# Kernel optimization log

Hardware: AMD Instinct MI355X
Metric: run time of the kernel (lower is better)

The kernel has to match this reference:

```python
import jax, jax.numpy as jnp
import numpy as np

N_NODES = 50000
N_EDGES = 800000
D_IN, D_HID, D_OUT = 128, 256, 256


def _sage_conv(x, src, dst, w_l, b_l, w_r, n_nodes):
    # PyG SAGEConv (mean aggr): out = lin_l(mean_{j in N(i)} x_j) + lin_r(x_i)
    # lin_l has bias, lin_r has no bias.
    msg_sum = jax.ops.segment_sum(x[src], dst, num_segments=n_nodes)  # [N, d]
    deg = jax.ops.segment_sum(jnp.ones_like(dst, dtype=x.dtype), dst, num_segments=n_nodes)
    agg = msg_sum / jnp.maximum(deg, 1.0)[:, None]
    return agg @ w_l.T + b_l + x @ w_r.T


def setup_inputs() -> dict:
    key = jax.random.key(0)
    ks = jax.random.split(key, 8)
    x = jax.random.normal(ks[0], (N_NODES, D_IN), dtype=jnp.float32)
    edge_index = jax.random.randint(ks[1], (2, N_EDGES), 0, N_NODES, dtype=jnp.int64)
    s1 = 1.0 / np.sqrt(D_IN)
    s2 = 1.0 / np.sqrt(D_HID)
    w_l1 = jax.random.uniform(ks[2], (D_HID, D_IN), jnp.float32, -s1, s1)
    b_l1 = jax.random.uniform(ks[3], (D_HID,), jnp.float32, -s1, s1)
    w_r1 = jax.random.uniform(ks[4], (D_HID, D_IN), jnp.float32, -s1, s1)
    w_l2 = jax.random.uniform(ks[5], (D_OUT, D_HID), jnp.float32, -s2, s2)
    b_l2 = jax.random.uniform(ks[6], (D_OUT,), jnp.float32, -s2, s2)
    w_r2 = jax.random.uniform(ks[7], (D_OUT, D_HID), jnp.float32, -s2, s2)
    return {"x": x, "edge_index": edge_index,
            "w_l1": w_l1, "b_l1": b_l1, "w_r1": w_r1,
            "w_l2": w_l2, "b_l2": b_l2, "w_r2": w_r2}


def reference(x, edge_index, w_l1, b_l1, w_r1, w_l2, b_l2, w_r2):
    src, dst = edge_index[0], edge_index[1]
    h = jax.nn.relu(_sage_conv(x, src, dst, w_l1, b_l1, w_r1, N_NODES))
    out = jax.nn.relu(_sage_conv(h, src, dst, w_l2, b_l2, w_r2, N_NODES))
    return out
```

## Files before the change

### kernel.cpp

```cpp
#include <hip/hip_runtime.h>
#include <hip/hip_fp16.h>
#include <stdint.h>

#define N_NODES 50000
#define N_EDGES 800000
#define BCAP 64
#define NPART 782
#define NSUB 16
#define SCAP 128

typedef _Float16 f16x8 __attribute__((ext_vector_type(8)));
typedef __attribute__((ext_vector_type(4))) float f32x4;

__device__ __forceinline__ unsigned short f2h(float f) {
    return __builtin_bit_cast(unsigned short, (_Float16)f);
}

__device__ __forceinline__ unsigned char f2fp8o(float v) {
    v = fminf(v, 440.f) + 0.015625f;
    unsigned int u = __builtin_bit_cast(unsigned int, v);
    u += 0x7FFFFu + ((u >> 20) & 1u);
    return (unsigned char)((u >> 20) - 960u);
}

__device__ __forceinline__ void load_lds16(const void* g, void* l) {
    __builtin_amdgcn_global_load_lds(
        (const __attribute__((address_space(1))) void*)(uintptr_t)g,
        (__attribute__((address_space(3))) void*)(unsigned int)(uintptr_t)l,
        16, 0, 0);
}

__global__ __launch_bounds__(256) void part_append_k(
    const int* __restrict__ src, const int* __restrict__ dst,
    int* __restrict__ pcnt, unsigned int* __restrict__ pbuf, int nedges)
{
    int t = blockIdx.x * 256 + threadIdx.x;
    int e0 = t * 4;
    if (e0 >= nedges) return;
    int4 s4 = *(const int4*)(src + e0);
    int4 d4 = *(const int4*)(dst + e0);

    int c0 = (d4.x >> 6) * NSUB + ((e0 + 0) & (NSUB - 1));
    int c1 = (d4.y >> 6) * NSUB + ((e0 + 1) & (NSUB - 1));
    int c2 = (d4.z >> 6) * NSUB + ((e0 + 2) & (NSUB - 1));
    int c3 = (d4.w >> 6) * NSUB + ((e0 + 3) & (NSUB - 1));

    int p0 = atomicAdd(&pcnt[c0 * 16], 1);
    int p1 = atomicAdd(&pcnt[c1 * 16], 1);
    int p2 = atomicAdd(&pcnt[c2 * 16], 1);
    int p3 = atomicAdd(&pcnt[c3 * 16], 1);

    if (p0 < SCAP) pbuf[(size_t)c0 * SCAP + p0] = ((unsigned)(d4.x & 63) << 16) | (unsigned)s4.x;
    if (p1 < SCAP) pbuf[(size_t)c1 * SCAP + p1] = ((unsigned)(d4.y & 63) << 16) | (unsigned)s4.y;
    if (p2 < SCAP) pbuf[(size_t)c2 * SCAP + p2] = ((unsigned)(d4.z & 63) << 16) | (unsigned)s4.z;
    if (p3 < SCAP) pbuf[(size_t)c3 * SCAP + p3] = ((unsigned)(d4.w & 63) << 16) | (unsigned)s4.w;
}

__global__ __launch_bounds__(256) void part_bucket_k(
    const int* __restrict__ pcnt, const unsigned int* __restrict__ pbuf,
    int* __restrict__ bucket, int* __restrict__ degtot, float* __restrict__ invdeg)
{
    __shared__ int lcnt[64];
    int part = blockIdx.x, tid = threadIdx.x;
    int wv = tid >> 6, lane = tid & 63;
    if (tid < 64) lcnt[tid] = 0;
    __syncthreads();
#pragma unroll
    for (int sub = wv; sub < NSUB; sub += 4) {
        int cidx = part * NSUB + sub;
        int n = pcnt[cidx * 16];
        if (n > SCAP) n = SCAP;
        const unsigned int* pb = pbuf + (size_t)cidx * SCAP;
        for (int i = lane; i < n; i += 64) {
            unsigned int en = pb[i];
            int dlow = (int)(en >> 16), s = (int)(en & 0xFFFFu);
            int p = atomicAdd(&lcnt[dlow], 1);
            if (p < BCAP) bucket[(size_t)(part * 64 + dlow) * BCAP + p] = s;
        }
    }
    __syncthreads();
    if (tid < 64) {
        int node = part * 64 + tid;
        if (node < N_NODES) {
            int c = lcnt[tid];
            degtot[node] = (c > BCAP) ? BCAP : c;
            invdeg[node] = 1.0f / (float)(c > 1 ? c : 1);
        }
    }
}

__global__ __launch_bounds__(256) void cvt_x_k(
    const float* __restrict__ x, unsigned short* __restrict__ dst)
{
    int tid = blockIdx.x * 256 + threadIdx.x;
    if (tid >= N_NODES * 32) return;
    int row = tid >> 5, c = (tid & 31) * 4;
    float4 v = *(const float4*)(x + (size_t)row * 128 + c);
    ushort4 o;
    o.x = f2h(v.x); o.y = f2h(v.y); o.z = f2h(v.z); o.w = f2h(v.w);
    *(ushort4*)(dst + (size_t)row * 256 + 128 + c) = o;
}

__global__ __launch_bounds__(256) void cvt_w_k(
    const float* __restrict__ wl, const float* __restrict__ wr,
    unsigned short* __restrict__ dst, int Keach)
{
    int tid = blockIdx.x * 256 + threadIdx.x;
    if (tid >= 256 * 2 * Keach) return;
    int n = tid / (2 * Keach), k = tid - n * 2 * Keach;
    float v = (k < Keach) ? wl[(size_t)n * Keach + k]
                          : wr[(size_t)n * Keach + (k - Keach)];
    dst[tid] = f2h(v);
}

__device__ __forceinline__ void acch4(__half2* a, uint4 u) {
    a[0] = __hadd2(a[0], __builtin_bit_cast(__half2, u.x));
    a[1] = __hadd2(a[1], __builtin_bit_cast(__half2, u.y));
    a[2] = __hadd2(a[2], __builtin_bit_cast(__half2, u.z));
    a[3] = __hadd2(a[3], __builtin_bit_cast(__half2, u.w));
}

__global__ __launch_bounds__(256) void agg1_k(
    const unsigned short* __restrict__ feat,
    const int* __restrict__ bucket, const int* __restrict__ degtot,
    const float* __restrict__ invdeg,
    unsigned short* __restrict__ outmsg)
{
    int wv = threadIdx.x >> 6, lane = threadIdx.x & 63;
    int node = blockIdx.x * 4 + wv;
    if (node >= N_NODES) return;
    int deg = degtot[node];
    int idx0 = bucket[(size_t)node * BCAP + lane];
    const int sub = lane >> 4;
    const int col = lane & 15;

    __half2 acc[4] = {};
    auto rowp = [&](int s) { return (const uint4*)(feat + (size_t)s * 256 + col * 8); };

    int j = 0;
    for (; j + 16 <= deg; j += 16) {
        int s0 = __shfl(idx0, j + sub),     s1 = __shfl(idx0, j + 4 + sub);
        int s2 = __shfl(idx0, j + 8 + sub), s3 = __shfl(idx0, j + 12 + sub);
        uint4 u0 = *rowp(s0), u1 = *rowp(s1), u2 = *rowp(s2), u3 = *rowp(s3);
        acch4(acc, u0); acch4(acc, u1); acch4(acc, u2); acch4(acc, u3);
    }
    for (; j + 8 <= deg; j += 8) {
        int s0 = __shfl(idx0, j + sub), s1 = __shfl(idx0, j + 4 + sub);
        uint4 u0 = *rowp(s0), u1 = *rowp(s1);
        acch4(acc, u0); acch4(acc, u1);
    }
    for (; j + 4 <= deg; j += 4) {
        uint4 u0 = *rowp(__shfl(idx0, j + sub));
        acch4(acc, u0);
    }
    if (j < deg) {
        int e = j + sub;
        int ec = (e < deg) ? e : (deg - 1);
        uint4 u0 = *rowp(__shfl(idx0, ec));
        if (e < deg) acch4(acc, u0);
    }
#pragma unroll
    for (int stride = 32; stride >= 16; stride >>= 1)
#pragma unroll
        for (int v = 0; v < 4; v++) {
            int t = __shfl_xor(__builtin_bit_cast(int, acc[v]), stride);
            acc[v] = __hadd2(acc[v], __builtin_bit_cast(__half2, t));
        }

    if (lane < 16) {
        float s = invdeg[node];
        unsigned int o[4];
#pragma unroll
        for (int v = 0; v < 4; v++) {
            float2 f = __half22float2(acc[v]);
            o[v] = (unsigned int)f2h(f.x * s) | ((unsigned int)f2h(f.y * s) << 16);
        }
        *(uint4*)(outmsg + (size_t)node * 256 + lane * 8) = make_uint4(o[0], o[1], o[2], o[3]);
    }
}

__device__ __forceinline__ void accf8pk(__half2* a, unsigned int w) {
    unsigned int ev = ((w & 0x00FF00FFu) << 7) + 0x20002000u;
    unsigned int od = ((w >> 1) & 0x7F807F80u) + 0x20002000u;
    a[0] = __hadd2(a[0], __builtin_bit_cast(__half2, ev));
    a[1] = __hadd2(a[1], __builtin_bit_cast(__half2, od));
}
__device__ __forceinline__ void accf8x16(__half2* a, uint4 u) {
    accf8pk(a + 0, u.x); accf8pk(a + 2, u.y); accf8pk(a + 4, u.z); accf8pk(a + 6, u.w);
}

__global__ __launch_bounds__(256) void agg2_k(
    const unsigned char* __restrict__ hf8,
    const int* __restrict__ bucket, const int* __restrict__ degtot,
    const float* __restrict__ invdeg,
    unsigned short* __restrict__ outmsg)
{
    int wv = threadIdx.x >> 6, lane = threadIdx.x & 63;
    int node = blockIdx.x * 4 + wv;
    if (node >= N_NODES) return;
    int deg = degtot[node];
    int idx0 = bucket[(size_t)node * BCAP + lane];
    const int sub = lane >> 4;
    const int col = lane & 15;

    __half2 acc[8] = {};
    auto rowp = [&](int s) { return (const uint4*)(hf8 + (size_t)s * 256 + col * 16); };

    int j = 0;
    for (; j + 16 <= deg; j += 16) {
        int s0 = __shfl(idx0, j + sub),     s1 = __shfl(idx0, j + 4 + sub);
        int s2 = __shfl(idx0, j + 8 + sub), s3 = __shfl(idx0, j + 12 + sub);
        uint4 u0 = *rowp(s0), u1 = *rowp(s1), u2 = *rowp(s2), u3 = *rowp(s3);
        accf8x16(acc, u0); accf8x16(acc, u1); accf8x16(acc, u2); accf8x16(acc, u3);
    }
    for (; j + 8 <= deg; j += 8) {
        int s0 = __shfl(idx0, j + sub), s1 = __shfl(idx0, j + 4 + sub);
        uint4 u0 = *rowp(s0), u1 = *rowp(s1);
        accf8x16(acc, u0); accf8x16(acc, u1);
    }
    for (; j + 4 <= deg; j += 4) {
        uint4 u0 = *rowp(__shfl(idx0, j + sub));
        accf8x16(acc, u0);
    }
    if (j < deg) {
        int e = j + sub;
        int ec = (e < deg) ? e : (deg - 1);
        uint4 u0 = *rowp(__shfl(idx0, ec));
        if (e < deg) accf8x16(acc, u0);
    }
#pragma unroll
    for (int stride = 32; stride >= 16; stride >>= 1)
#pragma unroll
        for (int v = 0; v < 8; v++) {
            int t = __shfl_xor(__builtin_bit_cast(int, acc[v]), stride);
            acc[v] = __hadd2(acc[v], __builtin_bit_cast(__half2, t));
        }

    if (lane < 16) {
        float s = invdeg[node];
        float bias = (deg > 0) ? 0.015625f : 0.0f;
        unsigned int o[8];
#pragma unroll
        for (int q = 0; q < 4; q++) {
            float2 ev = __half22float2(acc[2 * q]);
            float2 od = __half22float2(acc[2 * q + 1]);
            float d0 = ev.x * s - bias, d1 = od.x * s - bias;
            float d2 = ev.y * s - bias, d3 = od.y * s - bias;
            o[2 * q]     = (unsigned int)f2h(d0) | ((unsigned int)f2h(d1) << 16);
            o[2 * q + 1] = (unsigned int)f2h(d2) | ((unsigned int)f2h(d3) << 16);
        }
        unsigned short* wp = outmsg + (size_t)node * 512 + lane * 16;
        *(uint4*)(wp)     = make_uint4(o[0], o[1], o[2], o[3]);
        *(uint4*)(wp + 8) = make_uint4(o[4], o[5], o[6], o[7]);
    }
}

template <bool F16OUT, bool WRITE_FP8, int K>
__global__ __launch_bounds__(256) void gemm_k(
    const unsigned short* __restrict__ A, const unsigned short* __restrict__ W,
    const float* __restrict__ bias, void* __restrict__ outp, int outStride,
    unsigned char* __restrict__ hf8, int M)
{
    constexpr int NITER = K / 32;
    constexpr int KC = K / 8;
    __shared__ __align__(16) char smem[64 * K * 2];

    const int t = threadIdx.x;
    const int w = t >> 6, lane = t & 63;
    const int quad = lane >> 4, l15 = lane & 15;
    const int row0 = blockIdx.x * 128;
    const int col0 = blockIdx.y * 64;

    for (int c = t; c < 64 * KC; c += 256) {
        int col = c / KC;
        int kc  = (c % KC) ^ (col & 7);
        load_lds16(W + (size_t)(col0 + col) * K + kc * 8, smem + c * 16);
    }

    int r0 = row0 + w * 32 + l15;      if (r0 > M - 1) r0 = M - 1;
    int r1 = row0 + w * 32 + 16 + l15; if (r1 > M - 1) r1 = M - 1;
    const unsigned short* pA0 = A + (size_t)r0 * K + quad * 8;
    const unsigned short* pA1 = A + (size_t)r1 * K + quad * 8;

    f16x8 a0c, a1c, a0n, a1n;
    a0c = *(const f16x8*)(pA0);
    a1c = *(const f16x8*)(pA1);

    __syncthreads();

    const int qs = (quad * 16) ^ ((l15 & 7) << 4);
    const char* wp0 = smem + (size_t)(0 * 16 + l15) * (2 * K);
    const char* wp1 = smem + (size_t)(1 * 16 + l15) * (2 * K);
    const char* wp2 = smem + (size_t)(2 * 16 + l15) * (2 * K);
    const char* wp3 = smem + (size_t)(3 * 16 + l15) * (2 * K);

    f32x4 acc[2][4] = {};

    for (int i = 0; i < NITER; i++) {
        if (i + 1 < NITER) {
            a0n = *(const f16x8*)(pA0 + (i + 1) * 32);
            a1n = *(const f16x8*)(pA1 + (i + 1) * 32);
        }
        const int off = (i * 64) ^ qs;
        f16x8 b0 = *(const f16x8*)(wp0 + off);
        f16x8 b1 = *(const f16x8*)(wp1 + off);
        f16x8 b2 = *(const f16x8*)(wp2 + off);
        f16x8 b3 = *(const f16x8*)(wp3 + off);
        acc[0][0] = __builtin_amdgcn_mfma_f32_16x16x32_f16(a0c, b0, acc[0][0], 0, 0, 0);
        acc[1][0] = __builtin_amdgcn_mfma_f32_16x16x32_f16(a1c, b0, acc[1][0], 0, 0, 0);
        acc[0][1] = __builtin_amdgcn_mfma_f32_16x16x32_f16(a0c, b1, acc[0][1], 0, 0, 0);
        acc[1][1] = __builtin_amdgcn_mfma_f32_16x16x32_f16(a1c, b1, acc[1][1], 0, 0, 0);
        acc[0][2] = __builtin_amdgcn_mfma_f32_16x16x32_f16(a0c, b2, acc[0][2], 0, 0, 0);
        acc[1][2] = __builtin_amdgcn_mfma_f32_16x16x32_f16(a1c, b2, acc[1][2], 0, 0, 0);
        acc[0][3] = __builtin_amdgcn_mfma_f32_16x16x32_f16(a0c, b3, acc[0][3], 0, 0, 0);
        acc[1][3] = __builtin_amdgcn_mfma_f32_16x16x32_f16(a1c, b3, acc[1][3], 0, 0, 0);
        a0c = a0n; a1c = a1n;
    }

#pragma unroll
    for (int g = 0; g < 2; g++) {
#pragma unroll
        for (int tt = 0; tt < 4; tt++) {
            int col = col0 + tt * 16 + l15;
            float bv = bias[col];
#pragma unroll
            for (int i = 0; i < 4; i++) {
                int row = row0 + w * 32 + g * 16 + quad * 4 + i;
                if (row < M) {
                    float v = fmaxf(acc[g][tt][i] + bv, 0.f);
                    size_t off = (size_t)row * outStride + col;
                    if constexpr (F16OUT) ((unsigned short*)outp)[off] = f2h(v);
                    else                  ((float*)outp)[off] = v;
                    if constexpr (WRITE_FP8) hf8[(size_t)row * 256 + col] = f2fp8o(v);
                }
            }
        }
    }
}

extern "C" void kernel_launch(void* const* d_in, const int* in_sizes, int n_in,
                              void* d_out, int out_size, void* d_ws, size_t ws_size,
                              hipStream_t stream)
{
    const float* x   = (const float*)d_in[0];
    const int*   ei  = (const int*)d_in[1];
    const float* wl1 = (const float*)d_in[2];
    const float* bl1 = (const float*)d_in[3];
    const float* wr1 = (const float*)d_in[4];
    const float* wl2 = (const float*)d_in[5];
    const float* bl2 = (const float*)d_in[6];
    const float* wr2 = (const float*)d_in[7];
    float* out = (float*)d_out;
    const int* src = ei;
    const int* dst = ei + N_EDGES;

    char* ws = (char*)d_ws;
    size_t off = 0;
    auto alloc = [&](size_t bytes) -> void* {
        void* p = ws + off;
        off = (off + bytes + 255) & ~(size_t)255;
        return p;
    };
    int*            pcnt   = (int*)           alloc((size_t)NPART * NSUB * 16 * 4);
    unsigned int*   pbuf   = (unsigned int*)  alloc((size_t)NPART * NSUB * SCAP * 4);
    int*            bucket = (int*)           alloc((size_t)NPART * 64 * BCAP * 4);
    int*            degtot = (int*)           alloc((size_t)N_NODES * 4);
    float*          invdeg = (float*)         alloc((size_t)N_NODES * 4);
    unsigned short* Acat1  = (unsigned short*)alloc((size_t)N_NODES * 256 * 2);
    unsigned short* Acat2  = (unsigned short*)alloc((size_t)N_NODES * 512 * 2);
    unsigned char*  hf8    = (unsigned char*) alloc((size_t)N_NODES * 256);
    unsigned short* Wcat1  = (unsigned short*)alloc((size_t)256 * 256 * 2);
    unsigned short* Wcat2  = (unsigned short*)alloc((size_t)256 * 512 * 2);

    hipMemsetAsync(pcnt, 0, (size_t)NPART * NSUB * 16 * 4, stream);
    part_append_k<<<(N_EDGES / 4 + 255) / 256, 256, 0, stream>>>(src, dst, pcnt, pbuf, N_EDGES);
    part_bucket_k<<<NPART, 256, 0, stream>>>(pcnt, pbuf, bucket, degtot, invdeg);

    cvt_x_k<<<(N_NODES * 32 + 255) / 256, 256, 0, stream>>>(x, Acat1);
    cvt_w_k<<<(256 * 256 + 255) / 256, 256, 0, stream>>>(wl1, wr1, Wcat1, 128);
    cvt_w_k<<<(256 * 512 + 255) / 256, 256, 0, stream>>>(wl2, wr2, Wcat2, 256);

    agg1_k<<<(N_NODES + 3) / 4, 256, 0, stream>>>(
        Acat1 + 128, bucket, degtot, invdeg, Acat1);
    gemm_k<true, true, 256><<<dim3((N_NODES + 127) / 128, 4), 256, 0, stream>>>(
        Acat1, Wcat1, bl1, (void*)(Acat2 + 256), 512, hf8, N_NODES);

    agg2_k<<<(N_NODES + 3) / 4, 256, 0, stream>>>(
        hf8, bucket, degtot, invdeg, Acat2);
    gemm_k<false, false, 512><<<dim3((N_NODES + 127) / 128, 4), 256, 0, stream>>>(
        Acat2, Wcat2, bl2, (void*)out, 256, nullptr, N_NODES);
}
```

Before: 292.4 us.

## Enlarge GEMM row tile to 256, pre-swizzle W in LDS, deepen A prefetch

The GEMM kernel now gives each wave 64 rows instead of 32, so a block covers 256 rows by 64 columns. The W tile is stored in LDS in MFMA fragment order, so each lane reads B with one contiguous 16-byte load instead of XOR-swizzled addresses. A-fragment loads are prefetched two iterations ahead through a 4-deep register ring. The grid is reordered so column blocks are the fast dimension, which lets the blocks sharing the same A rows run close together for L2 reuse. The cost is higher register pressure from 16 accumulators and more A registers, which may reduce occupancy.

New measurement: 314.3 us. 7.5% more time.

```diff
diff --git a/kernel.cpp b/kernel.cpp
--- a/kernel.cpp
+++ b/kernel.cpp
@@ -262,72 +262,68 @@
     unsigned char* __restrict__ hf8, int M)
 {
     constexpr int NITER = K / 32;
-    constexpr int KC = K / 8;
-    __shared__ __align__(16) char smem[64 * K * 2];
+    __shared__ __align__(16) char smem[NITER * 4096];
 
     const int t = threadIdx.x;
-    const int w = t >> 6, lane = t & 63;
+    const int wv = t >> 6, lane = t & 63;
     const int quad = lane >> 4, l15 = lane & 15;
-    const int row0 = blockIdx.x * 128;
-    const int col0 = blockIdx.y * 64;
-
-    for (int c = t; c < 64 * KC; c += 256) {
-        int col = c / KC;
-        int kc  = (c % KC) ^ (col & 7);
-        load_lds16(W + (size_t)(col0 + col) * K + kc * 8, smem + c * 16);
-    }
-
-    int r0 = row0 + w * 32 + l15;      if (r0 > M - 1) r0 = M - 1;
-    int r1 = row0 + w * 32 + 16 + l15; if (r1 > M - 1) r1 = M - 1;
-    const unsigned short* pA0 = A + (size_t)r0 * K + quad * 8;
-    const unsigned short* pA1 = A + (size_t)r1 * K + quad * 8;
-
-    f16x8 a0c, a1c, a0n, a1n;
-    a0c = *(const f16x8*)(pA0);
-    a1c = *(const f16x8*)(pA1);
+    const int col0 = blockIdx.x * 64;
+    const int row0 = blockIdx.y * 256 + wv * 64;
+
+#pragma unroll
+    for (int n = 0; n < NITER; n++) {
+        int c = n * 256 + t;
+        int cl = c & 63, tt = (c >> 6) & 3, ki = c >> 8;
+        load_lds16(W + (size_t)(col0 + tt * 16 + (cl & 15)) * K + ki * 32 + (cl >> 4) * 8,
+                   smem + c * 16);
+    }
+
+    const unsigned short* pA[4];
+#pragma unroll
+    for (int rg = 0; rg < 4; rg++) {
+        int r = row0 + rg * 16 + l15;
+        if (r > M - 1) r = M - 1;
+        pA[rg] = A + (size_t)r * K + quad * 8;
+    }
+
+    f16x8 ab[4][4];
+#pragma unroll
+    for (int rg = 0; rg < 4; rg++) ab[0][rg] = *(const f16x8*)(pA[rg]);
+#pragma unroll
+    for (int rg = 0; rg < 4; rg++) ab[1][rg] = *(const f16x8*)(pA[rg] + 32);
 
     __syncthreads();
 
-    const int qs = (quad * 16) ^ ((l15 & 7) << 4);
-    const char* wp0 = smem + (size_t)(0 * 16 + l15) * (2 * K);
-    const char* wp1 = smem + (size_t)(1 * 16 + l15) * (2 * K);
-    const char* wp2 = smem + (size_t)(2 * 16 + l15) * (2 * K);
-    const char* wp3 = smem + (size_t)(3 * 16 + l15) * (2 * K);
-
-    f32x4 acc[2][4] = {};
-
+    f32x4 acc[4][4] = {};
+#pragma unroll
     for (int i = 0; i < NITER; i++) {
-        if (i + 1 < NITER) {
-            a0n = *(const f16x8*)(pA0 + (i + 1) * 32);
-            a1n = *(const f16x8*)(pA1 + (i + 1) * 32);
-        }
-        const int off = (i * 64) ^ qs;
-        f16x8 b0 = *(const f16x8*)(wp0 + off);
-        f16x8 b1 = *(const f16x8*)(wp1 + off);
-        f16x8 b2 = *(const f16x8*)(wp2 + off);
-        f16x8 b3 = *(const f16x8*)(wp3 + off);
-        acc[0][0] = __builtin_amdgcn_mfma_f32_16x16x32_f16(a0c, b0, acc[0][0], 0, 0, 0);
-        acc[1][0] = __builtin_amdgcn_mfma_f32_16x16x32_f16(a1c, b0, acc[1][0], 0, 0, 0);
-        acc[0][1] = __builtin_amdgcn_mfma_f32_16x16x32_f16(a0c, b1, acc[0][1], 0, 0, 0);
-        acc[1][1] = __builtin_amdgcn_mfma_f32_16x16x32_f16(a1c, b1, acc[1][1], 0, 0, 0);
-        acc[0][2] = __builtin_amdgcn_mfma_f32_16x16x32_f16(a0c, b2, acc[0][2], 0, 0, 0);
-        acc[1][2] = __builtin_amdgcn_mfma_f32_16x16x32_f16(a1c, b2, acc[1][2], 0, 0, 0);
-        acc[0][3] = __builtin_amdgcn_mfma_f32_16x16x32_f16(a0c, b3, acc[0][3], 0, 0, 0);
-        acc[1][3] = __builtin_amdgcn_mfma_f32_16x16x32_f16(a1c, b3, acc[1][3], 0, 0, 0);
-        a0c = a0n; a1c = a1n;
-    }
-
-#pragma unroll
-    for (int g = 0; g < 2; g++) {
+        if (i + 2 < NITER) {
+#pragma unroll
+            for (int rg = 0; rg < 4; rg++)
+                ab[(i + 2) & 3][rg] = *(const f16x8*)(pA[rg] + (i + 2) * 32);
+        }
+        const char* wb = smem + i * 4096 + lane * 16;
 #pragma unroll
         for (int tt = 0; tt < 4; tt++) {
-            int col = col0 + tt * 16 + l15;
-            float bv = bias[col];
-#pragma unroll
-            for (int i = 0; i < 4; i++) {
-                int row = row0 + w * 32 + g * 16 + quad * 4 + i;
+            f16x8 b = *(const f16x8*)(wb + tt * 1024);
+#pragma unroll
+            for (int rg = 0; rg < 4; rg++)
+                acc[rg][tt] = __builtin_amdgcn_mfma_f32_16x16x32_f16(
+                    ab[i & 3][rg], b, acc[rg][tt], 0, 0, 0);
+        }
+    }
+
+#pragma unroll
+    for (int tt = 0; tt < 4; tt++) {
+        int col = col0 + tt * 16 + l15;
+        float bv = bias[col];
+#pragma unroll
+        for (int rg = 0; rg < 4; rg++) {
+#pragma unroll
+            for (int ii = 0; ii < 4; ii++) {
+                int row = row0 + rg * 16 + quad * 4 + ii;
                 if (row < M) {
-                    float v = fmaxf(acc[g][tt][i] + bv, 0.f);
+                    float v = fmaxf(acc[rg][tt][ii] + bv, 0.f);
                     size_t off = (size_t)row * outStride + col;
                     if constexpr (F16OUT) ((unsigned short*)outp)[off] = f2h(v);
                     else                  ((float*)outp)[off] = v;
@@ -382,11 +378,11 @@
 
     agg1_k<<<(N_NODES + 3) / 4, 256, 0, stream>>>(
         Acat1 + 128, bucket, degtot, invdeg, Acat1);
-    gemm_k<true, true, 256><<<dim3((N_NODES + 127) / 128, 4), 256, 0, stream>>>(
+    gemm_k<true, true, 256><<<dim3(4, (N_NODES + 255) / 256), 256, 0, stream>>>(
         Acat1, Wcat1, bl1, (void*)(Acat2 + 256), 512, hf8, N_NODES);
 
     agg2_k<<<(N_NODES + 3) / 4, 256, 0, stream>>>(
         hf8, bucket, degtot, invdeg, Acat2);
-    gemm_k<false, false, 512><<<dim3((N_NODES + 127) / 128, 4), 256, 0, stream>>>(
+    gemm_k<false, false, 512><<<dim3(4, (N_NODES + 255) / 256), 256, 0, stream>>>(
         Acat2, Wcat2, bl2, (void*)out, 256, nullptr, N_NODES);
 }
```
